# Kernel tuning notes

Measured on AMD Instinct MI355X. Metric: run time of the kernel, lower is better.

## Reference

```python
import jax, jax.numpy as jnp
import numpy as np

NUM_GROUPS = 32
EPS = 1e-6


def group_norm(x, gamma, beta):
    # x: [b, c, h, w]
    b, c, h, w = x.shape
    xg = x.reshape(b, NUM_GROUPS, c // NUM_GROUPS, h, w)
    mean = xg.mean(axis=(2, 3, 4), keepdims=True)
    var = xg.var(axis=(2, 3, 4), keepdims=True)
    xn = ((xg - mean) * jax.lax.rsqrt(var + EPS)).reshape(b, c, h, w)
    return xn * gamma[None, :, None, None] + beta[None, :, None, None]


def conv1x1(x, w, bias):
    # 1x1 conv == channel-mixing matmul. x: [b,c,h,w], w: [co,ci]
    y = jnp.einsum('bchw,oc->bohw', x, w)
    return y + bias[None, :, None, None]


def setup_inputs() -> dict:
    key = jax.random.key(0)
    ks = jax.random.split(key, 10)
    B, C, H, W = 4, 512, 64, 64
    s = 1.0 / np.sqrt(C)
    inp = {
        'x': jax.random.normal(ks[0], (B, C, H, W), jnp.float32),
        'gamma': jnp.ones((C,), jnp.float32),
        'beta': jnp.zeros((C,), jnp.float32),
        'wq': jax.random.normal(ks[1], (C, C), jnp.float32) * s,
        'bq': jnp.zeros((C,), jnp.float32),
        'wk': jax.random.normal(ks[2], (C, C), jnp.float32) * s,
        'bk': jnp.zeros((C,), jnp.float32),
        'wv': jax.random.normal(ks[3], (C, C), jnp.float32) * s,
        'bv': jnp.zeros((C,), jnp.float32),
        'wo': jax.random.normal(ks[4], (C, C), jnp.float32) * s,
        'bo': jnp.zeros((C,), jnp.float32),
    }
    return inp


def reference(x, gamma, beta, wq, bq, wk, bk, wv, bv, wo, bo):
    b, c, h, w = x.shape
    h_ = group_norm(x, gamma, beta)
    q = conv1x1(h_, wq, bq).reshape(b, c, h * w)  # [b,c,n]
    k = conv1x1(h_, wk, bk).reshape(b, c, h * w)
    v = conv1x1(h_, wv, bv).reshape(b, c, h * w)
    scale = jnp.asarray(c, x.dtype) ** -0.5
    # scores: [b, n, n] = q^T k
    scores = jnp.einsum('bcn,bcm->bnm', q, k) * scale
    attn = jax.nn.softmax(scores, axis=2)
    # out: [b, c, n] = v @ attn^T  (h_[i] = sum_j attn[i,j] v[j])
    out = jnp.einsum('bnm,bcm->bcn', attn, v).reshape(b, c, h, w)
    out = conv1x1(out, wo, bo)
    return x + out
```

## Files before the change

### kernel.cpp

```cpp
#include <hip/hip_runtime.h>

typedef __bf16 bf16x8 __attribute__((ext_vector_type(8)));
typedef float f32x4 __attribute__((ext_vector_type(4)));
typedef unsigned short u16;

__device__ __forceinline__ u16 f2bf(float f) {
  unsigned int u = __builtin_bit_cast(unsigned int, f);
  u += 0x7fff + ((u >> 16) & 1);
  return (u16)(u >> 16);
}
__device__ __forceinline__ float bf2f(u16 s) {
  unsigned int u = ((unsigned int)s) << 16;
  return __builtin_bit_cast(float, u);
}
__device__ __forceinline__ void unp8(uint4 u, float* f) {
  f[0] = bf2f(u.x & 0xffff); f[1] = bf2f(u.x >> 16);
  f[2] = bf2f(u.y & 0xffff); f[3] = bf2f(u.y >> 16);
  f[4] = bf2f(u.z & 0xffff); f[5] = bf2f(u.z >> 16);
  f[6] = bf2f(u.w & 0xffff); f[7] = bf2f(u.w >> 16);
}
__device__ __forceinline__ uint4 pk8(const float* f) {
  uint4 u;
  u.x = (unsigned)f2bf(f[0]) | ((unsigned)f2bf(f[1]) << 16);
  u.y = (unsigned)f2bf(f[2]) | ((unsigned)f2bf(f[3]) << 16);
  u.z = (unsigned)f2bf(f[4]) | ((unsigned)f2bf(f[5]) << 16);
  u.w = (unsigned)f2bf(f[6]) | ((unsigned)f2bf(f[7]) << 16);
  return u;
}

__device__ __forceinline__ void gl_lds16(const u16* g, u16* l) {
  __builtin_amdgcn_global_load_lds(
      (const __attribute__((address_space(1))) void*)g,
      (__attribute__((address_space(3))) void*)l, 16, 0, 0);
}

template <int MODE>
__global__ __launch_bounds__(512, 2) void gemm_nt256(
    const u16* __restrict__ A, int lda, unsigned long long sA,
    const u16* __restrict__ Bt, int ldb, unsigned long long sB,
    u16* __restrict__ Cout, int ldc, unsigned long long sC,
    unsigned long long sSplit, int K, float alpha, int tn,
    const float* __restrict__ bias_col, float* __restrict__ psum) {
  __shared__ u16 lds[2][4][8192];

  const int t = threadIdx.x;
  const int lane = t & 63;
  const int w = t >> 6;
  const int bz = blockIdx.z;
  A  += (size_t)bz * sA + (size_t)blockIdx.y * K;
  Bt += (size_t)bz * sB + (size_t)blockIdx.y * K;
  Cout += (size_t)blockIdx.y * sSplit;

  const int nwg = gridDim.x;
  const int flat = blockIdx.x;
  const int wg = (flat & 7) * (nwg >> 3) + (flat >> 3);
  const int m0 = (wg / tn) * 256;
  const int n0 = (wg % tn) * 256;

  const int NKT = K >> 6;

  const int sr = lane >> 3;
  const int sc = ((lane & 7) ^ sr) * 8;
  const u16* gA = A  + (size_t)(m0 + w * 16 + sr) * lda + sc;
  const u16* gB = Bt + (size_t)(n0 + w * 16 + sr) * ldb + sc;
  const size_t a128 = (size_t)128 * lda, b128 = (size_t)128 * ldb;
  const size_t a8 = (size_t)8 * lda, b8 = (size_t)8 * ldb;
  const int lws = w * 1024;

  auto stage = [&](int slot, int region, int kt) {
    kt = kt < NKT ? kt : NKT - 1;
    u16* l = &lds[slot][region][lws];
    if (region < 2) {
      const u16* g = gA + (region ? a128 : 0) + (size_t)kt * 64;
      gl_lds16(g, l);
      gl_lds16(g + a8, l + 512);
    } else {
      const u16* g = gB + (region == 3 ? b128 : 0) + (size_t)kt * 64;
      gl_lds16(g, l);
      gl_lds16(g + b8, l + 512);
    }
  };

  const int wr = w >> 2, wc = w & 3;
  const int fr = lane & 15, kg = lane >> 4;
  const int frx = (fr & 7) << 4;

  f32x4 acc[8][4] = {};
  f32x4 sacc[8] = {};
  bf16x8 af[4][2], bq[2][2];
  union { u16 u[8]; bf16x8 v; } ou;
#pragma unroll
  for (int i = 0; i < 8; ++i) ou.u[i] = 0x3F80;
  const bf16x8 onesb = ou.v;

#define LDA_(s, qm)                                                            \
  {                                                                            \
    const u16* Ab = &lds[s][0][0];                                             \
    _Pragma("unroll") for (int m = 0; m < 4; ++m) {                            \
      const int R = wr * 128 + (qm) * 64 + m * 16 + fr;                        \
      _Pragma("unroll") for (int kk = 0; kk < 2; ++kk)                         \
          af[m][kk] = *reinterpret_cast<const bf16x8*>(                        \
              Ab + R * 64 + (((kk * 64 + kg * 16) ^ frx) >> 1));               \
    }                                                                          \
  }
#define LDB_(s, qn)                                                            \
  {                                                                            \
    const u16* Bb = &lds[s][2][0];                                             \
    _Pragma("unroll") for (int n = 0; n < 2; ++n) {                            \
      const int R = wc * 64 + (qn) * 32 + n * 16 + fr;                         \
      _Pragma("unroll") for (int kk = 0; kk < 2; ++kk)                         \
          bq[n][kk] = *reinterpret_cast<const bf16x8*>(                        \
              Bb + R * 64 + (((kk * 64 + kg * 16) ^ frx) >> 1));               \
    }                                                                          \
  }
#define PH(s, qm, qn, DOA, DOB, ss, rr, kt, VM)                                \
  {                                                                            \
    if (DOA) LDA_(s, qm)                                                       \
    if (DOB) LDB_(s, qn)                                                       \
    stage(ss, rr, kt);                                                         \
    __builtin_amdgcn_s_barrier();                                              \
    asm volatile("s_waitcnt lgkmcnt(0)" ::: "memory");                         \
    __builtin_amdgcn_s_setprio(1);                                             \
    _Pragma("unroll") for (int kk = 0; kk < 2; ++kk)                           \
    _Pragma("unroll") for (int m = 0; m < 4; ++m)                              \
    _Pragma("unroll") for (int n = 0; n < 2; ++n)                              \
        acc[(qm)*4 + m][(qn)*2 + n] = __builtin_amdgcn_mfma_f32_16x16x32_bf16( \
            af[m][kk], bq[n][kk], acc[(qm)*4 + m][(qn)*2 + n], 0, 0, 0);       \
    if (MODE == 2 && (DOA) && wc == 0) {                                       \
      _Pragma("unroll") for (int kk = 0; kk < 2; ++kk)                         \
      _Pragma("unroll") for (int m = 0; m < 4; ++m)                            \
          sacc[(qm)*4 + m] = __builtin_amdgcn_mfma_f32_16x16x32_bf16(          \
              af[m][kk], onesb, sacc[(qm)*4 + m], 0, 0, 0);                    \
    }                                                                          \
    __builtin_amdgcn_s_setprio(0);                                             \
    if (VM) asm volatile("s_waitcnt vmcnt(2)" ::: "memory");                   \
    __builtin_amdgcn_s_barrier();                                              \
  }

  stage(0, 0, 0); stage(0, 1, 0); stage(0, 2, 0); stage(0, 3, 0);
  stage(1, 0, 1);
  asm volatile("s_waitcnt vmcnt(2)" ::: "memory");
  __builtin_amdgcn_s_barrier();

  for (int j = 0; j < (NKT >> 1); ++j) {
    const int k1 = 2 * j + 1, k2 = 2 * j + 2, k3 = 2 * j + 3;
    PH(0, 0, 0, 1, 1, 1, 1, k1, 0)
    PH(0, 0, 1, 0, 1, 1, 2, k1, 0)
    PH(0, 1, 1, 1, 0, 1, 3, k1, 0)
    PH(0, 1, 0, 0, 1, 0, 0, k2, 1)
    PH(1, 0, 0, 1, 1, 0, 1, k2, 0)
    PH(1, 0, 1, 0, 1, 0, 2, k2, 0)
    PH(1, 1, 1, 1, 0, 0, 3, k2, 0)
    PH(1, 1, 0, 0, 1, 1, 0, k3, 1)
  }
#undef PH
#undef LDB_
#undef LDA_

  __syncthreads();
  u16* cs = &lds[0][0][0];
#pragma unroll
  for (int a = 0; a < 8; ++a) {
    const int row = wr * 128 + a * 16 + (kg << 2);
#pragma unroll
    for (int b = 0; b < 4; ++b) {
      const int col = wc * 64 + b * 16 + fr;
      float bc = 0.0f;
      if (MODE == 0 && bias_col) bc = bias_col[n0 + col];
#pragma unroll
      for (int r = 0; r < 4; ++r) {
        float v;
        if (MODE == 1) v = exp2f(acc[a][b][r] * alpha);
        else v = acc[a][b][r] * alpha + bc;
        cs[(row + r) * 256 + col] = f2bf(v);
      }
    }
  }
  __syncthreads();
  const size_t cbs = (size_t)bz * sC;
#pragma unroll
  for (int it = 0; it < 16; ++it) {
    const int off = (it * 512 + t) * 8;
    const int row = off >> 8, col = off & 255;
    *reinterpret_cast<uint4*>(&Cout[cbs + (size_t)(m0 + row) * ldc + (n0 + col)]) =
        *reinterpret_cast<const uint4*>(&cs[off]);
  }
  if (MODE == 2 && psum && wc == 0 && fr == 0) {
    const int Mrows = (nwg / tn) << 8;
    float* pp = psum + ((size_t)bz * gridDim.y + blockIdx.y) * Mrows + m0;
#pragma unroll
    for (int q = 0; q < 2; ++q)
#pragma unroll
      for (int m = 0; m < 4; ++m)
#pragma unroll
        for (int r = 0; r < 4; ++r)
          pp[wr * 128 + q * 64 + m * 16 + (kg << 2) + r] = sacc[q * 4 + m][r];
  }
}

template <bool OUT_F32>
__global__ __launch_bounds__(256) void gemm_nt(
    const u16* __restrict__ A, int lda, unsigned long long sA,
    const u16* __restrict__ Bt, int ldb, unsigned long long sB,
    void* __restrict__ Cout, int ldc, unsigned long long sC,
    int K, float alpha,
    const float* __restrict__ bias_row, const float* __restrict__ bias_col,
    const float* __restrict__ residual, unsigned long long sRes) {
  __shared__ u16 lds[128 * 128];
  u16* As = lds;
  u16* Bs = lds + 8192;

  const int t = threadIdx.x;
  const int bz = blockIdx.z;
  A  += (size_t)bz * sA;
  Bt += (size_t)bz * sB;
  const int m0 = blockIdx.x * 128;
  const int n0 = blockIdx.y * 128;

  const int lane = t & 63;
  const int w = t >> 6;

  const int srow = w * 32 + (lane >> 3);
  const int scol = (lane & 7) * 8;
  const u16* gA = A  + (size_t)(m0 + srow) * lda + scol;
  const u16* gB = Bt + (size_t)(n0 + srow) * ldb + scol;
  u16* lA = As + w * 2048;
  u16* lB = Bs + w * 2048;

  f32x4 acc[4][4] = {};
  const int wm = (w >> 1) * 64;
  const int wn = (w & 1) * 64;
  const int fr = lane & 15;
  const int kg = lane >> 4;

  for (int k0 = 0; k0 < K; k0 += 64) {
    __syncthreads();
#pragma unroll
    for (int i = 0; i < 4; ++i) {
      gl_lds16(gA + (size_t)(i * 8) * lda + k0, lA + i * 512);
      gl_lds16(gB + (size_t)(i * 8) * ldb + k0, lB + i * 512);
    }
    __syncthreads();

#pragma unroll
    for (int kk = 0; kk < 2; ++kk) {
      bf16x8 af[4], bfr[4];
#pragma unroll
      for (int m = 0; m < 4; ++m)
        af[m] = *reinterpret_cast<const bf16x8*>(
            &As[(wm + m * 16 + fr) * 64 + kk * 32 + kg * 8]);
#pragma unroll
      for (int n = 0; n < 4; ++n)
        bfr[n] = *reinterpret_cast<const bf16x8*>(
            &Bs[(wn + n * 16 + fr) * 64 + kk * 32 + kg * 8]);
#pragma unroll
      for (int m = 0; m < 4; ++m)
#pragma unroll
        for (int n = 0; n < 4; ++n)
          acc[m][n] = __builtin_amdgcn_mfma_f32_16x16x32_bf16(af[m], bfr[n], acc[m][n], 0, 0, 0);
    }
  }

  const size_t cbase = (size_t)bz * sC;
  const size_t rbase = (size_t)bz * sRes;
  const int rq = kg * 4;

  if (OUT_F32) {
    float* Cf = reinterpret_cast<float*>(Cout);
    float* lf = reinterpret_cast<float*>(lds);
#pragma unroll
    for (int h = 0; h < 2; ++h) {
      __syncthreads();
      if ((wm >> 6) == h) {
#pragma unroll
        for (int m = 0; m < 4; ++m)
#pragma unroll
          for (int n = 0; n < 4; ++n) {
            const float bc = bias_col ? bias_col[n0 + wn + n * 16 + fr] : 0.0f;
#pragma unroll
            for (int r = 0; r < 4; ++r)
              lf[(m * 16 + rq + r) * 128 + (wn + n * 16 + fr)] =
                  acc[m][n][r] * alpha + bc;
          }
      }
      __syncthreads();
#pragma unroll
      for (int it = 0; it < 8; ++it) {
        const int off = (it * 256 + t) * 4;
        const int row = off >> 7, col = off & 127;
        const int grow = m0 + h * 64 + row, gcol = n0 + col;
        float4 v = *reinterpret_cast<const float4*>(&lf[off]);
        if (bias_row) {
          const float br = bias_row[grow];
          v.x += br; v.y += br; v.z += br; v.w += br;
        }
        if (residual) {
          const float4 rx = *reinterpret_cast<const float4*>(
              &residual[rbase + (size_t)grow * ldc + gcol]);
          v.x += rx.x; v.y += rx.y; v.z += rx.z; v.w += rx.w;
        }
        *reinterpret_cast<float4*>(&Cf[cbase + (size_t)grow * ldc + gcol]) = v;
      }
    }
  } else {
    __syncthreads();
#pragma unroll
    for (int m = 0; m < 4; ++m) {
#pragma unroll
      for (int n = 0; n < 4; ++n) {
        const int gcol = n0 + wn + n * 16 + fr;
        const float bc = bias_col ? bias_col[gcol] : 0.0f;
#pragma unroll
        for (int r = 0; r < 4; ++r) {
          const int grow = m0 + wm + m * 16 + rq + r;
          float v = acc[m][n][r] * alpha + bc;
          if (bias_row) v += bias_row[grow];
          lds[(wm + m * 16 + rq + r) * 128 + (wn + n * 16 + fr)] = f2bf(v);
        }
      }
    }
    __syncthreads();
    u16* Cb = reinterpret_cast<u16*>(Cout);
#pragma unroll
    for (int j = 0; j < 8; ++j) {
      const int off = (j * 256 + t) * 8;
      const int row = off >> 7, col = off & 127;
      *reinterpret_cast<uint4*>(&Cb[cbase + (size_t)(m0 + row) * ldc + (n0 + col)]) =
          *reinterpret_cast<const uint4*>(&lds[off]);
    }
  }
}

__global__ __launch_bounds__(256) void groupnorm_k(
    const float* __restrict__ x, const float* __restrict__ gamma,
    const float* __restrict__ beta, u16* __restrict__ h_t, int C, int N) {
  const int g = blockIdx.x;
  const int b = blockIdx.y;
  const int t = threadIdx.x;
  const float* xb = x + ((size_t)b * C + g * 16) * N;

  float s = 0.f, q = 0.f;
  for (int c = 0; c < 16; ++c) {
    const float4* xr = reinterpret_cast<const float4*>(xb + (size_t)c * N);
    for (int j = t; j < N / 4; j += 256) {
      float4 v = xr[j];
      s += v.x + v.y + v.z + v.w;
      q += v.x * v.x + v.y * v.y + v.z * v.z + v.w * v.w;
    }
  }
#pragma unroll
  for (int o = 32; o > 0; o >>= 1) { s += __shfl_down(s, o); q += __shfl_down(q, o); }
  __shared__ float rs[4], rqs[4], stats[2];
  const int lane = t & 63, wid = t >> 6;
  if (lane == 0) { rs[wid] = s; rqs[wid] = q; }
  __syncthreads();
  if (t == 0) {
    float S = rs[0] + rs[1] + rs[2] + rs[3];
    float Q = rqs[0] + rqs[1] + rqs[2] + rqs[3];
    const float inv = 1.0f / (16.0f * (float)N);
    float mean = S * inv;
    float var = Q * inv - mean * mean;
    stats[0] = mean;
    stats[1] = rsqrtf(var + 1e-6f);
  }
  __syncthreads();
  const float mean = stats[0], rstd = stats[1];

  float gm[16], bt[16];
#pragma unroll
  for (int c = 0; c < 16; ++c) {
    gm[c] = gamma[g * 16 + c] * rstd;
    bt[c] = beta[g * 16 + c] - mean * gm[c];
  }
  u16* ho = h_t + (size_t)b * N * C + g * 16;
  for (int n = t; n < N; n += 256) {
    union { u16 us[16]; uint4 v4[2]; } pk;
#pragma unroll
    for (int c = 0; c < 16; ++c) {
      float v = xb[(size_t)c * N + n];
      pk.us[c] = f2bf(v * gm[c] + bt[c]);
    }
    uint4* dst = reinterpret_cast<uint4*>(ho + (size_t)n * C);
    dst[0] = pk.v4[0];
    dst[1] = pk.v4[1];
  }
}

__global__ __launch_bounds__(256) void wcvt(const float* __restrict__ src,
                                            u16* __restrict__ dst, int n) {
  const int i = (blockIdx.x * 256 + threadIdx.x) * 8;
  if (i >= n) return;
  const float4* s4 = reinterpret_cast<const float4*>(src + i);
  float4 a = s4[0], b = s4[1];
  float f[8] = {a.x, a.y, a.z, a.w, b.x, b.y, b.z, b.w};
  *reinterpret_cast<uint4*>(dst + i) = pk8(f);
}

__global__ __launch_bounds__(256) void bcat2(const float* __restrict__ a,
                                             const float* __restrict__ b,
                                             float* __restrict__ o, int n) {
  const int i = blockIdx.x * 256 + threadIdx.x;
  if (i < n) o[i] = a[i];
  else if (i < 2 * n) o[i] = b[i - n];
}

__global__ __launch_bounds__(256) void sumred(const float* __restrict__ psum,
                                              float* __restrict__ invl,
                                              int nt, int rows, int total) {
  const int i = blockIdx.x * 256 + threadIdx.x;
  if (i >= total) return;
  const int b = i / rows, n = i - b * rows;
  const float* p = psum + (size_t)b * nt * rows + n;
  float s = 0.f;
  for (int c = 0; c < nt; ++c) s += p[(size_t)c * rows];
  invl[i] = 1.0f / s;
}

__global__ __launch_bounds__(256) void reduce_pv(const u16* __restrict__ p,
                                                 const float* __restrict__ invl,
                                                 u16* __restrict__ o, int n) {
  const int i = (blockIdx.x * 256 + threadIdx.x) * 8;
  if (i >= n) return;
  const float il = invl[i >> 9];
  uint4 a = *reinterpret_cast<const uint4*>(p + i);
  uint4 b = *reinterpret_cast<const uint4*>(p + n + i);
  float fa[8], fb[8];
  unp8(a, fa); unp8(b, fb);
#pragma unroll
  for (int j = 0; j < 8; ++j) fa[j] = (fa[j] + fb[j]) * il;
  *reinterpret_cast<uint4*>(o + i) = pk8(fa);
}

__global__ __launch_bounds__(256) void scale_o(u16* __restrict__ o,
                                               const float* __restrict__ invl,
                                               int n) {
  const int i = (blockIdx.x * 256 + threadIdx.x) * 8;
  if (i >= n) return;
  const float il = invl[i >> 9];
  uint4 a = *reinterpret_cast<const uint4*>(o + i);
  float fa[8];
  unp8(a, fa);
#pragma unroll
  for (int j = 0; j < 8; ++j) fa[j] *= il;
  *reinterpret_cast<uint4*>(o + i) = pk8(fa);
}

extern "C" void kernel_launch(void* const* d_in, const int* in_sizes, int n_in,
                              void* d_out, int out_size, void* d_ws, size_t ws_size,
                              hipStream_t stream) {
  const float* x     = (const float*)d_in[0];
  const float* gamma = (const float*)d_in[1];
  const float* beta  = (const float*)d_in[2];
  const float* wq    = (const float*)d_in[3];
  const float* bq    = (const float*)d_in[4];
  const float* wk    = (const float*)d_in[5];
  const float* bk    = (const float*)d_in[6];
  const float* wv    = (const float*)d_in[7];
  const float* bv    = (const float*)d_in[8];
  const float* wo    = (const float*)d_in[9];
  const float* bo    = (const float*)d_in[10];

  const int B = 4, C = 512, N = 4096;
  const size_t NC = (size_t)N * C;
  const size_t NN = (size_t)N * N;
  const size_t CC = (size_t)C * C;

  char* ws = (char*)d_ws;
  size_t off = 0;
  auto alloc = [&](size_t bytes) {
    size_t r = off;
    off = (off + bytes + 255) & ~(size_t)255;
    return r;
  };
  u16* wq_b = (u16*)(ws + alloc(CC * 2));
  u16* wk_b = (u16*)(ws + alloc(CC * 2));
  u16* wv_b = (u16*)(ws + alloc(CC * 2));
  u16* wo_b = (u16*)(ws + alloc(CC * 2));
  float* bqk = (float*)(ws + alloc(1024 * 4));
  u16* h_t  = (u16*)(ws + alloc(B * NC * 2));
  u16* qk_t = (u16*)(ws + alloc(B * N * 1024 * 2));
  u16* v_cn = (u16*)(ws + alloc(B * NC * 2));
  u16* o_t  = (u16*)(ws + alloc(B * NC * 2));
  float* psum = (float*)(ws + alloc((size_t)B * 2 * N * 4));
  float* invl = (float*)(ws + alloc((size_t)B * N * 4));
  const size_t base_need = off;

  int s_batched = 0;
  u16* S;
  if (ws_size >= base_need + B * NN * 2) {
    S = (u16*)(ws + alloc(B * NN * 2));
    s_batched = 1;
  } else {
    S = (u16*)(ws + alloc(NN * 2));
  }
  u16* o_part = qk_t;

  wcvt<<<dim3(CC / 2048), 256, 0, stream>>>(wq, wq_b, (int)CC);
  wcvt<<<dim3(CC / 2048), 256, 0, stream>>>(wk, wk_b, (int)CC);
  wcvt<<<dim3(CC / 2048), 256, 0, stream>>>(wv, wv_b, (int)CC);
  wcvt<<<dim3(CC / 2048), 256, 0, stream>>>(wo, wo_b, (int)CC);
  bcat2<<<dim3(4), 256, 0, stream>>>(bq, bk, bqk, C);

  groupnorm_k<<<dim3(32, B), 256, 0, stream>>>(x, gamma, beta, h_t, C, N);

  gemm_nt256<0><<<dim3((N / 256) * (1024 / 256), 1, B), 512, 0, stream>>>(
      h_t, C, NC, wq_b, C, 0, qk_t, 1024, (unsigned long long)N * 1024, 0,
      C, 1.0f, 1024 / 256, bqk, nullptr);
  dim3 gv(C / 128, N / 128, B);
  gemm_nt<false><<<gv, 256, 0, stream>>>(wv_b, C, 0, h_t, C, NC, v_cn, N, NC,
                                         C, 1.0f, bv, nullptr, nullptr, 0);

  const float c1 = 0.06376694387439652f;
  if (s_batched) {
    gemm_nt256<1><<<dim3((N / 256) * (N / 256), 1, B), 512, 0, stream>>>(
        qk_t, 1024, (unsigned long long)N * 1024, qk_t + 512, 1024,
        (unsigned long long)N * 1024, S, N, NN, 0, C, c1, N / 256, nullptr, nullptr);
    gemm_nt256<2><<<dim3((N / 256) * (C / 256), 2, B), 512, 0, stream>>>(
        S, N, NN, v_cn, N, NC, o_part, C, NC, (unsigned long long)B * NC,
        N / 2, 1.0f, C / 256, nullptr, psum);
    sumred<<<dim3(B * N / 256), 256, 0, stream>>>(psum, invl, 2, N, B * N);
    reduce_pv<<<dim3((int)(B * NC / 2048)), 256, 0, stream>>>(
        o_part, invl, o_t, (int)(B * NC));
  } else {
    for (int b = 0; b < B; ++b) {
      gemm_nt256<1><<<dim3((N / 256) * (N / 256), 1, 1), 512, 0, stream>>>(
          qk_t + (size_t)b * N * 1024, 1024, 0, qk_t + (size_t)b * N * 1024 + 512,
          1024, 0, S, N, 0, 0, C, c1, N / 256, nullptr, nullptr);
      gemm_nt256<2><<<dim3((N / 256) * (C / 256), 1, 1), 512, 0, stream>>>(
          S, N, 0, v_cn + (size_t)b * NC, N, 0, o_t + (size_t)b * NC, C, 0, 0,
          N, 1.0f, C / 256, nullptr, psum + (size_t)b * N);
    }
    sumred<<<dim3(B * N / 256), 256, 0, stream>>>(psum, invl, 1, N, B * N);
    scale_o<<<dim3((int)(B * NC / 2048)), 256, 0, stream>>>(o_t, invl, (int)(B * NC));
  }

  dim3 gf(C / 128, N / 128, B);
  gemm_nt<true><<<gf, 256, 0, stream>>>(wo_b, C, 0, o_t, C, NC, d_out, N, NC,
                                        C, 1.0f, bo, nullptr, x, NC);
}
```

Baseline: 317.6 us.

## Merge small launches, drop sumred/bcat kernels, reorder tile mapping in gemm_nt256

Merges the four weight conversions into one 2D-grid kernel. Removes the bias-concat kernel by letting the QK projection GEMM read bq and bk directly, and removes the row-sum reduction kernel by having reduce_pv and scale_o compute the inverse softmax denominator from psum inline. The aim is to cut the cost of several tiny kernel launches. It also changes the workgroup-to-tile mapping so adjacent workgroups pair two M tiles per N tile, which is meant to improve L2 reuse.

```diff
diff --git a/kernel.cpp b/kernel.cpp
--- a/kernel.cpp
+++ b/kernel.cpp
@@ -40,7 +40,8 @@
     const u16* __restrict__ Bt, int ldb, unsigned long long sB,
     u16* __restrict__ Cout, int ldc, unsigned long long sC,
     unsigned long long sSplit, int K, float alpha, int tn,
-    const float* __restrict__ bias_col, float* __restrict__ psum) {
+    const float* __restrict__ bias_col, const float* __restrict__ bias_col2,
+    float* __restrict__ psum) {
   __shared__ u16 lds[2][4][8192];
 
   const int t = threadIdx.x;
@@ -54,8 +55,11 @@
   const int nwg = gridDim.x;
   const int flat = blockIdx.x;
   const int wg = (flat & 7) * (nwg >> 3) + (flat >> 3);
-  const int m0 = (wg / tn) * 256;
-  const int n0 = (wg % tn) * 256;
+  const int tt = tn << 1;
+  const int p  = wg / tt;
+  const int rr = wg - p * tt;
+  const int m0 = (p * 2 + (rr & 1)) * 256;
+  const int n0 = (rr >> 1) * 256;
 
   const int NKT = K >> 6;
 
@@ -113,11 +117,11 @@
               Bb + R * 64 + (((kk * 64 + kg * 16) ^ frx) >> 1));               \
     }                                                                          \
   }
-#define PH(s, qm, qn, DOA, DOB, ss, rr, kt, VM)                                \
+#define PH(s, qm, qn, DOA, DOB, ss, rr_, kt, VM)                               \
   {                                                                            \
     if (DOA) LDA_(s, qm)                                                       \
     if (DOB) LDB_(s, qn)                                                       \
-    stage(ss, rr, kt);                                                         \
+    stage(ss, rr_, kt);                                                        \
     __builtin_amdgcn_s_barrier();                                              \
     asm volatile("s_waitcnt lgkmcnt(0)" ::: "memory");                         \
     __builtin_amdgcn_s_setprio(1);                                             \
@@ -166,7 +170,10 @@
     for (int b = 0; b < 4; ++b) {
       const int col = wc * 64 + b * 16 + fr;
       float bc = 0.0f;
-      if (MODE == 0 && bias_col) bc = bias_col[n0 + col];
+      if (MODE == 0 && bias_col) {
+        const int gc = n0 + col;
+        bc = (bias_col2 && gc >= 512) ? bias_col2[gc - 512] : bias_col[gc & 511];
+      }
 #pragma unroll
       for (int r = 0; r < 4; ++r) {
         float v;
@@ -386,57 +393,44 @@
   }
 }
 
-__global__ __launch_bounds__(256) void wcvt(const float* __restrict__ src,
-                                            u16* __restrict__ dst, int n) {
+__global__ __launch_bounds__(256) void wcvt4(
+    const float* __restrict__ s0, const float* __restrict__ s1,
+    const float* __restrict__ s2, const float* __restrict__ s3,
+    u16* __restrict__ dst, int n) {
   const int i = (blockIdx.x * 256 + threadIdx.x) * 8;
   if (i >= n) return;
+  const float* src = (blockIdx.y == 0) ? s0 : (blockIdx.y == 1) ? s1
+                     : (blockIdx.y == 2) ? s2 : s3;
   const float4* s4 = reinterpret_cast<const float4*>(src + i);
   float4 a = s4[0], b = s4[1];
   float f[8] = {a.x, a.y, a.z, a.w, b.x, b.y, b.z, b.w};
-  *reinterpret_cast<uint4*>(dst + i) = pk8(f);
-}
-
-__global__ __launch_bounds__(256) void bcat2(const float* __restrict__ a,
-                                             const float* __restrict__ b,
-                                             float* __restrict__ o, int n) {
-  const int i = blockIdx.x * 256 + threadIdx.x;
-  if (i < n) o[i] = a[i];
-  else if (i < 2 * n) o[i] = b[i - n];
-}
-
-__global__ __launch_bounds__(256) void sumred(const float* __restrict__ psum,
-                                              float* __restrict__ invl,
-                                              int nt, int rows, int total) {
-  const int i = blockIdx.x * 256 + threadIdx.x;
-  if (i >= total) return;
-  const int b = i / rows, n = i - b * rows;
-  const float* p = psum + (size_t)b * nt * rows + n;
-  float s = 0.f;
-  for (int c = 0; c < nt; ++c) s += p[(size_t)c * rows];
-  invl[i] = 1.0f / s;
+  *reinterpret_cast<uint4*>(dst + (size_t)blockIdx.y * n + i) = pk8(f);
 }
 
 __global__ __launch_bounds__(256) void reduce_pv(const u16* __restrict__ p,
-                                                 const float* __restrict__ invl,
+                                                 const float* __restrict__ psum,
                                                  u16* __restrict__ o, int n) {
   const int i = (blockIdx.x * 256 + threadIdx.x) * 8;
   if (i >= n) return;
-  const float il = invl[i >> 9];
+  const int row = i >> 9;
+  const int b = row >> 12, nn = row & 4095;
+  const float il = 1.0f / (psum[(size_t)(b * 2) * 4096 + nn] +
+                           psum[(size_t)(b * 2 + 1) * 4096 + nn]);
   uint4 a = *reinterpret_cast<const uint4*>(p + i);
-  uint4 b = *reinterpret_cast<const uint4*>(p + n + i);
+  uint4 bb = *reinterpret_cast<const uint4*>(p + n + i);
   float fa[8], fb[8];
-  unp8(a, fa); unp8(b, fb);
+  unp8(a, fa); unp8(bb, fb);
 #pragma unroll
   for (int j = 0; j < 8; ++j) fa[j] = (fa[j] + fb[j]) * il;
   *reinterpret_cast<uint4*>(o + i) = pk8(fa);
 }
 
 __global__ __launch_bounds__(256) void scale_o(u16* __restrict__ o,
-                                               const float* __restrict__ invl,
+                                               const float* __restrict__ psum,
                                                int n) {
   const int i = (blockIdx.x * 256 + threadIdx.x) * 8;
   if (i >= n) return;
-  const float il = invl[i >> 9];
+  const float il = 1.0f / psum[i >> 9];
   uint4 a = *reinterpret_cast<const uint4*>(o + i);
   float fa[8];
   unp8(a, fa);
@@ -476,13 +470,11 @@
   u16* wk_b = (u16*)(ws + alloc(CC * 2));
   u16* wv_b = (u16*)(ws + alloc(CC * 2));
   u16* wo_b = (u16*)(ws + alloc(CC * 2));
-  float* bqk = (float*)(ws + alloc(1024 * 4));
   u16* h_t  = (u16*)(ws + alloc(B * NC * 2));
   u16* qk_t = (u16*)(ws + alloc(B * N * 1024 * 2));
   u16* v_cn = (u16*)(ws + alloc(B * NC * 2));
   u16* o_t  = (u16*)(ws + alloc(B * NC * 2));
   float* psum = (float*)(ws + alloc((size_t)B * 2 * N * 4));
-  float* invl = (float*)(ws + alloc((size_t)B * N * 4));
   const size_t base_need = off;
 
   int s_batched = 0;
@@ -495,17 +487,15 @@
   }
   u16* o_part = qk_t;
 
-  wcvt<<<dim3(CC / 2048), 256, 0, stream>>>(wq, wq_b, (int)CC);
-  wcvt<<<dim3(CC / 2048), 256, 0, stream>>>(wk, wk_b, (int)CC);
-  wcvt<<<dim3(CC / 2048), 256, 0, stream>>>(wv, wv_b, (int)CC);
-  wcvt<<<dim3(CC / 2048), 256, 0, stream>>>(wo, wo_b, (int)CC);
-  bcat2<<<dim3(4), 256, 0, stream>>>(bq, bk, bqk, C);
+  (void)wk_b; (void)wv_b;
+
+  wcvt4<<<dim3(CC / 2048, 4), 256, 0, stream>>>(wq, wk, wv, wo, wq_b, (int)CC);
 
   groupnorm_k<<<dim3(32, B), 256, 0, stream>>>(x, gamma, beta, h_t, C, N);
 
   gemm_nt256<0><<<dim3((N / 256) * (1024 / 256), 1, B), 512, 0, stream>>>(
       h_t, C, NC, wq_b, C, 0, qk_t, 1024, (unsigned long long)N * 1024, 0,
-      C, 1.0f, 1024 / 256, bqk, nullptr);
+      C, 1.0f, 1024 / 256, bq, bk, nullptr);
   dim3 gv(C / 128, N / 128, B);
   gemm_nt<false><<<gv, 256, 0, stream>>>(wv_b, C, 0, h_t, C, NC, v_cn, N, NC,
                                          C, 1.0f, bv, nullptr, nullptr, 0);
@@ -514,24 +504,23 @@
   if (s_batched) {
     gemm_nt256<1><<<dim3((N / 256) * (N / 256), 1, B), 512, 0, stream>>>(
         qk_t, 1024, (unsigned long long)N * 1024, qk_t + 512, 1024,
-        (unsigned long long)N * 1024, S, N, NN, 0, C, c1, N / 256, nullptr, nullptr);
+        (unsigned long long)N * 1024, S, N, NN, 0, C, c1, N / 256,
+        nullptr, nullptr, nullptr);
     gemm_nt256<2><<<dim3((N / 256) * (C / 256), 2, B), 512, 0, stream>>>(
         S, N, NN, v_cn, N, NC, o_part, C, NC, (unsigned long long)B * NC,
-        N / 2, 1.0f, C / 256, nullptr, psum);
-    sumred<<<dim3(B * N / 256), 256, 0, stream>>>(psum, invl, 2, N, B * N);
+        N / 2, 1.0f, C / 256, nullptr, nullptr, psum);
     reduce_pv<<<dim3((int)(B * NC / 2048)), 256, 0, stream>>>(
-        o_part, invl, o_t, (int)(B * NC));
+        o_part, psum, o_t, (int)(B * NC));
   } else {
     for (int b = 0; b < B; ++b) {
       gemm_nt256<1><<<dim3((N / 256) * (N / 256), 1, 1), 512, 0, stream>>>(
           qk_t + (size_t)b * N * 1024, 1024, 0, qk_t + (size_t)b * N * 1024 + 512,
-          1024, 0, S, N, 0, 0, C, c1, N / 256, nullptr, nullptr);
+          1024, 0, S, N, 0, 0, C, c1, N / 256, nullptr, nullptr, nullptr);
       gemm_nt256<2><<<dim3((N / 256) * (C / 256), 1, 1), 512, 0, stream>>>(
           S, N, 0, v_cn + (size_t)b * NC, N, 0, o_t + (size_t)b * NC, C, 0, 0,
-          N, 1.0f, C / 256, nullptr, psum + (size_t)b * N);
-    }
-    sumred<<<dim3(B * N / 256), 256, 0, stream>>>(psum, invl, 1, N, B * N);
-    scale_o<<<dim3((int)(B * NC / 2048)), 256, 0, stream>>>(o_t, invl, (int)(B * NC));
+          N, 1.0f, C / 256, nullptr, nullptr, psum + (size_t)b * N);
+    }
+    scale_o<<<dim3((int)(B * NC / 2048)), 256, 0, stream>>>(o_t, psum, (int)(B * NC));
   }
 
   dim3 gf(C / 128, N / 128, B);
```

Result: faster. 306.3 us (-3.6%).
